# Performance work log

Hardware: AMD Instinct MI355X
Metric: run time of the kernel (lower is better)

## Reference

```python
import jax, jax.numpy as jnp
import numpy as np


def setup_inputs() -> dict:
    key = jax.random.key(0)
    k1, k2 = jax.random.split(key)
    x = jax.random.normal(k1, (32, 32, 32, 256), dtype=jnp.float32)
    mean = jnp.zeros((1,), dtype=jnp.float32)
    stddev = jnp.ones((1,), dtype=jnp.float32)
    embeddings = jax.random.normal(k2, (64, 512), dtype=jnp.float32)  # [embedding_dim, num_embeddings]
    return {"x": x, "mean": mean, "stddev": stddev, "embeddings": embeddings}


def _divide_no_nan(a, b):
    safe = jnp.where(b == 0, jnp.ones_like(b), b)
    return jnp.where(b == 0, jnp.zeros_like(a), a / safe)


def reference(x, mean, stddev, embeddings):
    b, h, w, c = x.shape
    embedding_dim, num_embeddings = embeddings.shape

    standardised = _divide_no_nan(x, stddev) - mean            # [b,h,w,c]
    standardised = jnp.transpose(standardised, (0, 3, 1, 2)).reshape(b, c, h * w)  # b c (h w)
    flat = standardised.reshape(-1, embedding_dim)             # [N, d], N = b*c*hw/d

    dist = (jnp.sum(flat * flat, axis=1, keepdims=True)
            + jnp.sum(embeddings * embeddings, axis=0)
            - 2.0 * (flat @ embeddings))                       # [N, K]
    discretised = jnp.argmin(dist, axis=1)                     # [N]

    # one-hot @ embeddings.T == row gather from embeddings.T
    quantised = jnp.take(embeddings.T, discretised, axis=0)    # [N, d]
    quantised = quantised.reshape(b, c, h * w)
    quantised = jnp.transpose(quantised.reshape(b, c, h, w), (0, 2, 3, 1))  # [b,h,w,c]

    discretised_out = discretised.reshape(-1, c)

    quantised = (quantised + mean) * stddev
    quantised = x + jax.lax.stop_gradient(quantised - x)       # straight-through
    return quantised, discretised_out
```

## Files before the change

### kernel.cpp

```cpp
#include <hip/hip_runtime.h>


typedef _Float16 f16;
typedef _Float16 f16x8 __attribute__((ext_vector_type(8)));
typedef float    f32x4 __attribute__((ext_vector_type(4)));

#define NELEM0 8388608
#define FLTMAX 3.402823466e38f
#define WS_NEED 270336

__device__ __forceinline__ void gload_lds16(const void* g, void* l) {
    __builtin_amdgcn_global_load_lds(
        (const __attribute__((address_space(1))) void*)g,
        (__attribute__((address_space(3))) void*)l, 16, 0, 0);
}

__device__ __forceinline__ int swz(int row, int koff) {
    return row * 128 + (koff ^ ((row & 7) << 3));
}

__global__ void prep_kernel(const float* __restrict__ emb, const float* __restrict__ meanp,
                            const float* __restrict__ sdp, f16* __restrict__ ecvt,
                            float* __restrict__ e2p, float* __restrict__ embt) {
    const int code = (blockIdx.x >> 2) * 256 + threadIdx.x;
    const int dc   = blockIdx.x & 3;
    const float mean = meanp[0];
    const float sd   = sdp[0];
    float s = 0.0f;
    #pragma unroll
    for (int j = 0; j < 16; ++j) {
        const int d = dc * 16 + j;
        float v = emb[d * 512 + code];
        s = fmaf(v, v, s);
        f16 h = (f16)v;
        f16 l = (f16)(v - (float)h);
        const int gg = (d >> 3) ^ (code & 7);
        const int e  = d & 7;
        ecvt[code * 128 + gg * 8 + e]      = h;
        ecvt[code * 128 + 64 + gg * 8 + e] = l;
        embt[code * 64 + d] = (v + mean) * sd;
    }
    e2p[dc * 512 + code] = s;
}

__global__ __launch_bounds__(256, 4)
void vq_main(const float* __restrict__ x, const float* __restrict__ meanp,
             const float* __restrict__ sdp, const f16* __restrict__ ecvt,
             const float* __restrict__ e2p, const float* __restrict__ embt,
             float* __restrict__ out, float* __restrict__ outIdx)
{
    __shared__ __align__(16) f16 es[2][64 * 128];
    __shared__ float e2s[512];
    __shared__ int   kbs[128];

    const int tid  = threadIdx.x;
    const int lane = tid & 63;
    const int wid  = tid >> 6;
    const int lr   = lane & 15;
    const int lk   = lane >> 4;

    const int blk   = blockIdx.x;
    const int chalf = blk & 1;
    const int g     = (blk >> 1) & 15;
    const int b     = blk >> 5;

    const float sd   = sdp[0];
    const bool  sdz  = (sd == 0.0f);
    const float sinv = sdz ? 0.0f : (1.0f / sd);
    const float mean = meanp[0];

    const size_t xslab = (size_t)b * 262144 + (size_t)g * 16384;
    const int c0 = chalf * 128 + wid * 32;

    #pragma unroll
    for (int i = 0; i < 4; ++i)
        gload_lds16(ecvt + i * 2048 + tid * 8, &es[0][i * 2048 + tid * 8]);

    f16x8 ah[2][2], al[2][2];
    #pragma unroll
    for (int s = 0; s < 2; ++s) {
        const float* rp = x + xslab + c0 + s * 16 + lr;
        #pragma unroll
        for (int ks = 0; ks < 2; ++ks)
            #pragma unroll
            for (int j = 0; j < 8; ++j) {
                float v  = rp[(ks * 32 + lk * 8 + j) * 256];
                float sv = fmaf(v, sinv, -mean);
                f16 h = (f16)sv;
                ah[s][ks][j] = h;
                al[s][ks][j] = (f16)(sv - (float)h);
            }
    }

    {
        e2s[tid] = ((e2p[tid] + e2p[512 + tid]) + e2p[1024 + tid]) + e2p[1536 + tid];
        const int t2 = 256 + tid;
        e2s[t2]  = ((e2p[t2]  + e2p[512 + t2])  + e2p[1024 + t2])  + e2p[1536 + t2];
    }
    __syncthreads();

    float bestv[8];
    int   besti[8];
    #pragma unroll
    for (int s = 0; s < 8; ++s) { bestv[s] = FLTMAX; besti[s] = 0; }

    for (int ch = 0; ch < 8; ++ch) {
        const int cur = ch & 1;
        const f16* eb = &es[cur][0];

        if (ch < 7) {
            #pragma unroll
            for (int i = 0; i < 4; ++i)
                gload_lds16(ecvt + (ch + 1) * 8192 + i * 2048 + tid * 8,
                            &es[cur ^ 1][i * 2048 + tid * 8]);
        }

        #pragma unroll
        for (int cf = 0; cf < 4; ++cf) {
            const int rowB = cf * 16 + lr;
            f16x8 bh0 = *reinterpret_cast<const f16x8*>(&eb[swz(rowB, lk * 8)]);
            f16x8 bh1 = *reinterpret_cast<const f16x8*>(&eb[swz(rowB, 32 + lk * 8)]);
            f16x8 bl0 = *reinterpret_cast<const f16x8*>(&eb[swz(rowB, 64 + lk * 8)]);
            f16x8 bl1 = *reinterpret_cast<const f16x8*>(&eb[swz(rowB, 96 + lk * 8)]);
            const int codeg = ch * 64 + cf * 16 + lr;
            const float e2v = e2s[codeg];
            #pragma unroll
            for (int s = 0; s < 2; ++s) {
                f32x4 a0 = (f32x4){0.f, 0.f, 0.f, 0.f};
                f32x4 a1 = (f32x4){0.f, 0.f, 0.f, 0.f};
                a0 = __builtin_amdgcn_mfma_f32_16x16x32_f16(ah[s][0], bh0, a0, 0, 0, 0);
                a0 = __builtin_amdgcn_mfma_f32_16x16x32_f16(ah[s][1], bh1, a0, 0, 0, 0);
                a0 = __builtin_amdgcn_mfma_f32_16x16x32_f16(ah[s][0], bl0, a0, 0, 0, 0);
                a1 = __builtin_amdgcn_mfma_f32_16x16x32_f16(ah[s][1], bl1, a1, 0, 0, 0);
                a1 = __builtin_amdgcn_mfma_f32_16x16x32_f16(al[s][0], bh0, a1, 0, 0, 0);
                a1 = __builtin_amdgcn_mfma_f32_16x16x32_f16(al[s][1], bh1, a1, 0, 0, 0);
                #pragma unroll
                for (int r = 0; r < 4; ++r) {
                    float vd = fmaf(-2.0f, a0[r] + a1[r], e2v);
                    const int si = s * 4 + r;
                    if (vd < bestv[si]) { bestv[si] = vd; besti[si] = codeg; }
                }
            }
        }

        __syncthreads();
    }

    #pragma unroll
    for (int si = 0; si < 8; ++si) {
        float v = bestv[si]; int i = besti[si];
        #pragma unroll
        for (int m = 1; m < 16; m <<= 1) {
            float v2 = __shfl_xor(v, m, 64);
            int   i2 = __shfl_xor(i, m, 64);
            if (v2 < v || (v2 == v && i2 < i)) { v = v2; i = i2; }
        }
        bestv[si] = v; besti[si] = i;
    }
    if (lr == 0) {
        #pragma unroll
        for (int s = 0; s < 2; ++s)
            #pragma unroll
            for (int r = 0; r < 4; ++r)
                kbs[wid * 32 + s * 16 + lk * 4 + r] = besti[s * 4 + r];
    }
    __syncthreads();

    {
        const int c_ = tid & 127;
        const int dh = tid >> 7;
        const int k  = kbs[c_];
        const float* qrow = embt + k * 64 + dh * 32;
        float* op = out + xslab + (size_t)(dh * 32) * 256 + chalf * 128 + c_;
        #pragma unroll
        for (int q4 = 0; q4 < 8; ++q4) {
            f32x4 qq = *reinterpret_cast<const f32x4*>(&qrow[q4 * 4]);
            #pragma unroll
            for (int j = 0; j < 4; ++j)
                op[(q4 * 4 + j) * 256] = qq[j];
        }
    }
    if (tid < 128)
        outIdx[(size_t)(b * 256 + chalf * 128 + tid) * 16 + g] = (float)kbs[tid];
}

__global__ __launch_bounds__(512, 2)
void vq_fallback(const float* __restrict__ x, const float* __restrict__ meanp,
                 const float* __restrict__ sdp, const float* __restrict__ emb,
                 float* __restrict__ out, float* __restrict__ outIdx)
{
    __shared__ __align__(16) f16 xa[128 * 128];
    __shared__ __align__(16) f16 es2[128 * 128];
    __shared__ float e2s[512];
    __shared__ float red_v[4][128];
    __shared__ int   red_i[4][128];
    __shared__ int   kb[128];

    const int tid  = threadIdx.x;
    const int lane = tid & 63;
    const int wid  = tid >> 6;
    const int wr   = wid >> 2;
    const int wc   = wid & 3;
    const int lr   = lane & 15;
    const int lk   = lane >> 4;

    const int blk   = blockIdx.x;
    const int chalf = blk & 1;
    const int g     = (blk >> 1) & 15;
    const int b     = blk >> 5;

    const float mean = meanp[0];
    const float sd   = sdp[0];
    const bool  sdz  = (sd == 0.0f);
    const float safe = sdz ? 1.0f : sd;

    const int xbase = b * 262144 + g * 16384 + chalf * 128;

    {
        const int c_ = tid & 127;
        const int dq = tid >> 7;
        const float* src = x + xbase + c_;
        #pragma unroll
        for (int jv = 0; jv < 2; ++jv) {
            f16x8 hi, lo;
            #pragma unroll
            for (int e = 0; e < 8; ++e) {
                int d = dq * 16 + jv * 8 + e;
                float v = src[d * 256];
                float s = (sdz ? 0.0f : v / safe) - mean;
                f16 h = (f16)s;
                hi[e] = h;
                lo[e] = (f16)(s - (float)h);
            }
            *reinterpret_cast<f16x8*>(&xa[swz(c_, dq * 16 + jv * 8)])      = hi;
            *reinterpret_cast<f16x8*>(&xa[swz(c_, 64 + dq * 16 + jv * 8)]) = lo;
        }
    }
    {
        float s = 0.0f;
        for (int d = 0; d < 64; ++d) {
            float v = emb[d * 512 + tid];
            s = fmaf(v, v, s);
        }
        e2s[tid] = s;
    }

    float bestv[16];
    int   besti[16];
    #pragma unroll
    for (int s = 0; s < 16; ++s) { bestv[s] = FLTMAX; besti[s] = 0; }

    for (int ch = 0; ch < 4; ++ch) {
        __syncthreads();
        {
            const int cl = tid & 127;
            const int dq = tid >> 7;
            const float* srcE = emb + ch * 128 + cl;
            #pragma unroll
            for (int jv = 0; jv < 2; ++jv) {
                f16x8 hi, lo;
                #pragma unroll
                for (int e = 0; e < 8; ++e) {
                    int d = dq * 16 + jv * 8 + e;
                    float v = srcE[d * 512];
                    f16 h = (f16)v;
                    hi[e] = h;
                    lo[e] = (f16)(v - (float)h);
                }
                *reinterpret_cast<f16x8*>(&es2[swz(cl, dq * 16 + jv * 8)])      = hi;
                *reinterpret_cast<f16x8*>(&es2[swz(cl, 64 + dq * 16 + jv * 8)]) = lo;
            }
        }
        __syncthreads();

        f32x4 acc[4][2];
        #pragma unroll
        for (int fi = 0; fi < 4; ++fi)
            #pragma unroll
            for (int fj = 0; fj < 2; ++fj)
                acc[fi][fj] = (f32x4){0.f, 0.f, 0.f, 0.f};

        #pragma unroll
        for (int t = 0; t < 3; ++t) {
            const int ah2 = (t == 2) ? 1 : 0;
            const int eh2 = (t == 1) ? 1 : 0;
            #pragma unroll
            for (int dh2 = 0; dh2 < 2; ++dh2) {
                const int kB = eh2 * 64 + dh2 * 32 + lk * 8;
                const int kA = ah2 * 64 + dh2 * 32 + lk * 8;
                f16x8 bf[2], af[4];
                #pragma unroll
                for (int fj = 0; fj < 2; ++fj)
                    bf[fj] = *reinterpret_cast<const f16x8*>(
                        &es2[swz(wc * 32 + fj * 16 + lr, kB)]);
                #pragma unroll
                for (int fi = 0; fi < 4; ++fi)
                    af[fi] = *reinterpret_cast<const f16x8*>(
                        &xa[swz(wr * 64 + fi * 16 + lr, kA)]);
                #pragma unroll
                for (int fi = 0; fi < 4; ++fi)
                    #pragma unroll
                    for (int fj = 0; fj < 2; ++fj)
                        acc[fi][fj] = __builtin_amdgcn_mfma_f32_16x16x32_f16(
                            af[fi], bf[fj], acc[fi][fj], 0, 0, 0);
            }
        }

        #pragma unroll
        for (int fj = 0; fj < 2; ++fj) {
            const int codeg = ch * 128 + wc * 32 + fj * 16 + lr;
            const float e2v = e2s[codeg];
            #pragma unroll
            for (int fi = 0; fi < 4; ++fi)
                #pragma unroll
                for (int r = 0; r < 4; ++r) {
                    float vd = fmaf(-2.0f, acc[fi][fj][r], e2v);
                    const int s = fi * 4 + r;
                    if (vd < bestv[s]) { bestv[s] = vd; besti[s] = codeg; }
                }
        }
    }

    #pragma unroll
    for (int s = 0; s < 16; ++s) {
        float v = bestv[s]; int i = besti[s];
        #pragma unroll
        for (int m = 1; m < 16; m <<= 1) {
            float v2 = __shfl_xor(v, m, 64);
            int   i2 = __shfl_xor(i, m, 64);
            if (v2 < v || (v2 == v && i2 < i)) { v = v2; i = i2; }
        }
        bestv[s] = v; besti[s] = i;
    }
    if (lr == 0) {
        #pragma unroll
        for (int fi = 0; fi < 4; ++fi)
            #pragma unroll
            for (int r = 0; r < 4; ++r) {
                int row = wr * 64 + fi * 16 + lk * 4 + r;
                red_v[wc][row] = bestv[fi * 4 + r];
                red_i[wc][row] = besti[fi * 4 + r];
            }
    }
    __syncthreads();
    if (tid < 128) {
        float bv = red_v[0][tid]; int bi = red_i[0][tid];
        #pragma unroll
        for (int w2 = 1; w2 < 4; ++w2) {
            float v = red_v[w2][tid]; int i = red_i[w2][tid];
            if (v < bv || (v == bv && i < bi)) { bv = v; bi = i; }
        }
        kb[tid] = bi;
    }
    __syncthreads();

    float* out_ = out + xbase;
    #pragma unroll 4
    for (int i = 0; i < 16; ++i) {
        int lin = i * 512 + tid;
        int c_  = lin & 127;
        int d   = lin >> 7;
        float q = emb[d * 512 + kb[c_]];
        out_[d * 256 + c_] = (q + mean) * sd;
    }
    if (tid < 128) {
        int n = (b * 256 + chalf * 128 + tid) * 16 + g;
        outIdx[n] = (float)kb[tid];
    }
}

extern "C" void kernel_launch(void* const* d_in, const int* in_sizes, int n_in,
                              void* d_out, int out_size, void* d_ws, size_t ws_size,
                              hipStream_t stream) {
    const float* x    = (const float*)d_in[0];
    const float* mean = (const float*)d_in[1];
    const float* sd   = (const float*)d_in[2];
    const float* emb  = (const float*)d_in[3];
    float* out    = (float*)d_out;
    float* outIdx = out + NELEM0;

    if (ws_size >= (size_t)WS_NEED) {
        f16*   ecvt = (f16*)d_ws;
        float* e2p  = (float*)((char*)d_ws + 131072);
        float* embt = (float*)((char*)d_ws + 139264);
        prep_kernel<<<dim3(8), dim3(256), 0, stream>>>(emb, mean, sd, ecvt, e2p, embt);
        vq_main<<<dim3(1024), dim3(256), 0, stream>>>(x, mean, sd, ecvt, e2p, embt, out, outIdx);
    } else {
        vq_fallback<<<dim3(1024), dim3(512), 0, stream>>>(x, mean, sd, emb, out, outIdx);
    }
}
```

Before: 46.65 us.

## Switch distance GEMM to 32x32x16 MFMA with codebook norm folded into accumulator

Replaces the 16x16x32 MFMA tiling with 32x32x16 tiles that process 32 codes per chunk over 16 chunks. The -0.5*|e|^2 term is precomputed in the prep kernel as an f16 hi/lo pair and injected through an extra MFMA with a ones vector, which turns the argmin into an argmax with no per-element fma. The async global_load_lds double buffering is replaced by register prefetch followed by LDS stores, and the swizzle now XORs over 16 groups. The aim is fewer MFMA issues and less epilogue VALU work, at the cost of more accumulator registers and synchronous LDS writes.

```diff
diff --git a/kernel.cpp b/kernel.cpp
--- a/kernel.cpp
+++ b/kernel.cpp
@@ -2,62 +2,67 @@
 
 
 typedef _Float16 f16;
-typedef _Float16 f16x8 __attribute__((ext_vector_type(8)));
-typedef float    f32x4 __attribute__((ext_vector_type(4)));
+typedef _Float16 f16x8  __attribute__((ext_vector_type(8)));
+typedef float    f32x4  __attribute__((ext_vector_type(4)));
+typedef float    f32x16 __attribute__((ext_vector_type(16)));
 
 #define NELEM0 8388608
 #define FLTMAX 3.402823466e38f
 #define WS_NEED 270336
 
-__device__ __forceinline__ void gload_lds16(const void* g, void* l) {
-    __builtin_amdgcn_global_load_lds(
-        (const __attribute__((address_space(1))) void*)g,
-        (__attribute__((address_space(3))) void*)l, 16, 0, 0);
-}
-
-__device__ __forceinline__ int swz(int row, int koff) {
-    return row * 128 + (koff ^ ((row & 7) << 3));
-}
-
 __global__ void prep_kernel(const float* __restrict__ emb, const float* __restrict__ meanp,
                             const float* __restrict__ sdp, f16* __restrict__ ecvt,
-                            float* __restrict__ e2p, float* __restrict__ embt) {
-    const int code = (blockIdx.x >> 2) * 256 + threadIdx.x;
-    const int dc   = blockIdx.x & 3;
+                            f16* __restrict__ e2q, float* __restrict__ embt) {
+    __shared__ float e2part[4][64];
+    const int tid  = threadIdx.x;
+    const int code = blockIdx.x * 64 + (tid & 63);
+    const int q    = tid >> 6;
     const float mean = meanp[0];
     const float sd   = sdp[0];
     float s = 0.0f;
     #pragma unroll
     for (int j = 0; j < 16; ++j) {
-        const int d = dc * 16 + j;
+        const int d = q * 16 + j;
         float v = emb[d * 512 + code];
         s = fmaf(v, v, s);
         f16 h = (f16)v;
         f16 l = (f16)(v - (float)h);
-        const int gg = (d >> 3) ^ (code & 7);
-        const int e  = d & 7;
-        ecvt[code * 128 + gg * 8 + e]      = h;
-        ecvt[code * 128 + 64 + gg * 8 + e] = l;
+        const int sh = (d >> 3) ^ (code & 15);
+        const int sl = ((d >> 3) + 8) ^ (code & 15);
+        ecvt[code * 128 + sh * 8 + (d & 7)] = h;
+        ecvt[code * 128 + sl * 8 + (d & 7)] = l;
         embt[code * 64 + d] = (v + mean) * sd;
     }
-    e2p[dc * 512 + code] = s;
+    e2part[q][tid & 63] = s;
+    __syncthreads();
+    if (q == 0) {
+        const int c_ = tid & 63;
+        float e2 = ((e2part[0][c_] + e2part[1][c_]) + e2part[2][c_]) + e2part[3][c_];
+        float t  = -0.5f * e2;
+        f16 th = (f16)t;
+        f16 tl = (f16)(t - (float)th);
+        f16* dst = e2q + code * 8;
+        dst[0] = th; dst[1] = tl;
+        #pragma unroll
+        for (int e = 2; e < 8; ++e) dst[e] = (f16)0.0f;
+    }
 }
 
 __global__ __launch_bounds__(256, 4)
 void vq_main(const float* __restrict__ x, const float* __restrict__ meanp,
              const float* __restrict__ sdp, const f16* __restrict__ ecvt,
-             const float* __restrict__ e2p, const float* __restrict__ embt,
+             const f16* __restrict__ e2q, const float* __restrict__ embt,
              float* __restrict__ out, float* __restrict__ outIdx)
 {
-    __shared__ __align__(16) f16 es[2][64 * 128];
-    __shared__ float e2s[512];
-    __shared__ int   kbs[128];
+    __shared__ __align__(16) f16 es[2][4096];
+    __shared__ __align__(16) f16 e2s[4096];
+    __shared__ int kbs[128];
 
     const int tid  = threadIdx.x;
     const int lane = tid & 63;
     const int wid  = tid >> 6;
-    const int lr   = lane & 15;
-    const int lk   = lane >> 4;
+    const int lrow = lane & 31;
+    const int kh   = lane >> 5;
 
     const int blk   = blockIdx.x;
     const int chalf = blk & 1;
@@ -72,97 +77,100 @@
     const size_t xslab = (size_t)b * 262144 + (size_t)g * 16384;
     const int c0 = chalf * 128 + wid * 32;
 
-    #pragma unroll
-    for (int i = 0; i < 4; ++i)
-        gload_lds16(ecvt + i * 2048 + tid * 8, &es[0][i * 2048 + tid * 8]);
-
-    f16x8 ah[2][2], al[2][2];
-    #pragma unroll
-    for (int s = 0; s < 2; ++s) {
-        const float* rp = x + xslab + c0 + s * 16 + lr;
-        #pragma unroll
-        for (int ks = 0; ks < 2; ++ks)
-            #pragma unroll
-            for (int j = 0; j < 8; ++j) {
-                float v  = rp[(ks * 32 + lk * 8 + j) * 256];
+    f16x8 axh[4], axl[4];
+    {
+        const float* rp = x + xslab + c0 + lrow;
+        #pragma unroll
+        for (int p = 0; p < 4; ++p)
+            #pragma unroll
+            for (int e = 0; e < 8; ++e) {
+                const int d = p * 16 + kh * 8 + e;
+                float v  = rp[d * 256];
                 float sv = fmaf(v, sinv, -mean);
                 f16 h = (f16)sv;
-                ah[s][ks][j] = h;
-                al[s][ks][j] = (f16)(sv - (float)h);
+                axh[p][e] = h;
+                axl[p][e] = (f16)(sv - (float)h);
             }
     }
-
-    {
-        e2s[tid] = ((e2p[tid] + e2p[512 + tid]) + e2p[1024 + tid]) + e2p[1536 + tid];
-        const int t2 = 256 + tid;
-        e2s[t2]  = ((e2p[t2]  + e2p[512 + t2])  + e2p[1024 + t2])  + e2p[1536 + t2];
-    }
+    f16x8 aone;
+    #pragma unroll
+    for (int e = 0; e < 8; ++e)
+        aone[e] = (kh == 0 && e < 2) ? (f16)1.0f : (f16)0.0f;
+
+    #pragma unroll
+    for (int i = 0; i < 2; ++i)
+        *reinterpret_cast<f16x8*>(&e2s[(i * 256 + tid) * 8]) =
+            *reinterpret_cast<const f16x8*>(&e2q[(i * 256 + tid) * 8]);
+    f16x8 pre0 = *reinterpret_cast<const f16x8*>(&ecvt[tid * 8]);
+    f16x8 pre1 = *reinterpret_cast<const f16x8*>(&ecvt[2048 + tid * 8]);
+    *reinterpret_cast<f16x8*>(&es[0][tid * 8])        = pre0;
+    *reinterpret_cast<f16x8*>(&es[0][2048 + tid * 8]) = pre1;
     __syncthreads();
 
-    float bestv[8];
-    int   besti[8];
-    #pragma unroll
-    for (int s = 0; s < 8; ++s) { bestv[s] = FLTMAX; besti[s] = 0; }
-
-    for (int ch = 0; ch < 8; ++ch) {
+    float bestv[16];
+    int   besti[16];
+    #pragma unroll
+    for (int r = 0; r < 16; ++r) { bestv[r] = -FLTMAX; besti[r] = 0; }
+
+    for (int ch = 0; ch < 16; ++ch) {
         const int cur = ch & 1;
         const f16* eb = &es[cur][0];
 
-        if (ch < 7) {
-            #pragma unroll
-            for (int i = 0; i < 4; ++i)
-                gload_lds16(ecvt + (ch + 1) * 8192 + i * 2048 + tid * 8,
-                            &es[cur ^ 1][i * 2048 + tid * 8]);
-        }
-
-        #pragma unroll
-        for (int cf = 0; cf < 4; ++cf) {
-            const int rowB = cf * 16 + lr;
-            f16x8 bh0 = *reinterpret_cast<const f16x8*>(&eb[swz(rowB, lk * 8)]);
-            f16x8 bh1 = *reinterpret_cast<const f16x8*>(&eb[swz(rowB, 32 + lk * 8)]);
-            f16x8 bl0 = *reinterpret_cast<const f16x8*>(&eb[swz(rowB, 64 + lk * 8)]);
-            f16x8 bl1 = *reinterpret_cast<const f16x8*>(&eb[swz(rowB, 96 + lk * 8)]);
-            const int codeg = ch * 64 + cf * 16 + lr;
-            const float e2v = e2s[codeg];
-            #pragma unroll
-            for (int s = 0; s < 2; ++s) {
-                f32x4 a0 = (f32x4){0.f, 0.f, 0.f, 0.f};
-                f32x4 a1 = (f32x4){0.f, 0.f, 0.f, 0.f};
-                a0 = __builtin_amdgcn_mfma_f32_16x16x32_f16(ah[s][0], bh0, a0, 0, 0, 0);
-                a0 = __builtin_amdgcn_mfma_f32_16x16x32_f16(ah[s][1], bh1, a0, 0, 0, 0);
-                a0 = __builtin_amdgcn_mfma_f32_16x16x32_f16(ah[s][0], bl0, a0, 0, 0, 0);
-                a1 = __builtin_amdgcn_mfma_f32_16x16x32_f16(ah[s][1], bl1, a1, 0, 0, 0);
-                a1 = __builtin_amdgcn_mfma_f32_16x16x32_f16(al[s][0], bh0, a1, 0, 0, 0);
-                a1 = __builtin_amdgcn_mfma_f32_16x16x32_f16(al[s][1], bh1, a1, 0, 0, 0);
-                #pragma unroll
-                for (int r = 0; r < 4; ++r) {
-                    float vd = fmaf(-2.0f, a0[r] + a1[r], e2v);
-                    const int si = s * 4 + r;
-                    if (vd < bestv[si]) { bestv[si] = vd; besti[si] = codeg; }
-                }
-            }
-        }
-
+        if (ch < 15) {
+            pre0 = *reinterpret_cast<const f16x8*>(&ecvt[(ch + 1) * 4096 + tid * 8]);
+            pre1 = *reinterpret_cast<const f16x8*>(&ecvt[(ch + 1) * 4096 + 2048 + tid * 8]);
+        }
+
+        f32x16 acc = (f32x16){0.f,0.f,0.f,0.f, 0.f,0.f,0.f,0.f,
+                              0.f,0.f,0.f,0.f, 0.f,0.f,0.f,0.f};
+        {
+            const f16x8 be2 = *reinterpret_cast<const f16x8*>(&e2s[(ch * 32 + lrow) * 8]);
+            acc = __builtin_amdgcn_mfma_f32_32x32x16_f16(aone, be2, acc, 0, 0, 0);
+        }
+        #pragma unroll
+        for (int p = 0; p < 4; ++p) {
+            const f16x8 bp = *reinterpret_cast<const f16x8*>(
+                &eb[lrow * 128 + (((p * 2 + kh) ^ (lrow & 15)) << 3)]);
+            acc = __builtin_amdgcn_mfma_f32_32x32x16_f16(axh[p], bp, acc, 0, 0, 0);
+            acc = __builtin_amdgcn_mfma_f32_32x32x16_f16(axl[p], bp, acc, 0, 0, 0);
+        }
+        #pragma unroll
+        for (int p = 0; p < 4; ++p) {
+            const f16x8 bp = *reinterpret_cast<const f16x8*>(
+                &eb[lrow * 128 + ((((p * 2 + kh) + 8) ^ (lrow & 15)) << 3)]);
+            acc = __builtin_amdgcn_mfma_f32_32x32x16_f16(axh[p], bp, acc, 0, 0, 0);
+        }
+
+        const int codeg = ch * 32 + lrow;
+        #pragma unroll
+        for (int r = 0; r < 16; ++r) {
+            if (acc[r] > bestv[r]) { bestv[r] = acc[r]; besti[r] = codeg; }
+        }
+
+        if (ch < 15) {
+            *reinterpret_cast<f16x8*>(&es[cur ^ 1][tid * 8])        = pre0;
+            *reinterpret_cast<f16x8*>(&es[cur ^ 1][2048 + tid * 8]) = pre1;
+        }
         __syncthreads();
     }
 
     #pragma unroll
-    for (int si = 0; si < 8; ++si) {
-        float v = bestv[si]; int i = besti[si];
-        #pragma unroll
-        for (int m = 1; m < 16; m <<= 1) {
+    for (int r = 0; r < 16; ++r) {
+        float v = bestv[r]; int i = besti[r];
+        #pragma unroll
+        for (int m = 1; m < 32; m <<= 1) {
             float v2 = __shfl_xor(v, m, 64);
             int   i2 = __shfl_xor(i, m, 64);
-            if (v2 < v || (v2 == v && i2 < i)) { v = v2; i = i2; }
-        }
-        bestv[si] = v; besti[si] = i;
-    }
-    if (lr == 0) {
-        #pragma unroll
-        for (int s = 0; s < 2; ++s)
-            #pragma unroll
-            for (int r = 0; r < 4; ++r)
-                kbs[wid * 32 + s * 16 + lk * 4 + r] = besti[s * 4 + r];
+            if (v2 > v || (v2 == v && i2 < i)) { v = v2; i = i2; }
+        }
+        bestv[r] = v; besti[r] = i;
+    }
+    if (lrow == 0) {
+        #pragma unroll
+        for (int r = 0; r < 16; ++r) {
+            const int row = (r & 3) + 8 * (r >> 2) + 4 * kh;
+            kbs[wid * 32 + row] = besti[r];
+        }
     }
     __syncthreads();
 
@@ -182,6 +190,10 @@
     }
     if (tid < 128)
         outIdx[(size_t)(b * 256 + chalf * 128 + tid) * 16 + g] = (float)kbs[tid];
+}
+
+__device__ __forceinline__ int swz(int row, int koff) {
+    return row * 128 + (koff ^ ((row & 7) << 3));
 }
 
 __global__ __launch_bounds__(512, 2)
@@ -381,10 +393,10 @@
 
     if (ws_size >= (size_t)WS_NEED) {
         f16*   ecvt = (f16*)d_ws;
-        float* e2p  = (float*)((char*)d_ws + 131072);
+        f16*   e2q  = (f16*)((char*)d_ws + 131072);
         float* embt = (float*)((char*)d_ws + 139264);
-        prep_kernel<<<dim3(8), dim3(256), 0, stream>>>(emb, mean, sd, ecvt, e2p, embt);
-        vq_main<<<dim3(1024), dim3(256), 0, stream>>>(x, mean, sd, ecvt, e2p, embt, out, outIdx);
+        prep_kernel<<<dim3(8), dim3(256), 0, stream>>>(emb, mean, sd, ecvt, e2q, embt);
+        vq_main<<<dim3(1024), dim3(256), 0, stream>>>(x, mean, sd, ecvt, e2q, embt, out, outIdx);
     } else {
         vq_fallback<<<dim3(1024), dim3(512), 0, stream>>>(x, mean, sd, emb, out, outIdx);
     }
```

After: 51.46 us. 1.1x slower.
